# Optimization experiments

Measured on AMD Instinct MI355X. Metric: run time of the kernel, lower is better.

Reference implementation:

```python
import jax, jax.numpy as jnp
import numpy as np

E = 768      # embed_size
H = 12       # num_heads inside each nn.MultiheadAttention
G = 4        # num_groups
D = E // H   # per-head dim = 64


def setup_inputs() -> dict:
    key = jax.random.key(0)
    ks = jax.random.split(key, 20)
    s = 0.02
    B, S = 2, 2048
    inp = {
        "query": jax.random.normal(ks[0], (B, S, E), jnp.float32),
        "key":   jax.random.normal(ks[1], (B, S, E), jnp.float32),
        "value": jax.random.normal(ks[2], (B, S, E), jnp.float32),
        # outer projections (query_group_proj / key_proj / value_proj)
        "Wqg": jax.random.normal(ks[3], (E, E), jnp.float32) * s,
        "bqg": jnp.zeros((E,), jnp.float32),
        "Wk":  jax.random.normal(ks[4], (E, E), jnp.float32) * s,
        "bk":  jnp.zeros((E,), jnp.float32),
        "Wv":  jax.random.normal(ks[5], (E, E), jnp.float32) * s,
        "bv":  jnp.zeros((E,), jnp.float32),
        # per-group MultiheadAttention params (in_proj split into q/k/v, out_proj)
        "Wq_in": jax.random.normal(ks[6], (G, E, E), jnp.float32) * s,
        "bq_in": jnp.zeros((G, E), jnp.float32),
        "Wk_in": jax.random.normal(ks[7], (G, E, E), jnp.float32) * s,
        "bk_in": jnp.zeros((G, E), jnp.float32),
        "Wv_in": jax.random.normal(ks[8], (G, E, E), jnp.float32) * s,
        "bv_in": jnp.zeros((G, E), jnp.float32),
        "Wout":  jax.random.normal(ks[9], (G, E, E), jnp.float32) * s,
        "bout":  jnp.zeros((G, E), jnp.float32),
    }
    return inp


def reference(query, key, value, Wqg, bqg, Wk, bk, Wv, bv,
              Wq_in, bq_in, Wk_in, bk_in, Wv_in, bv_in, Wout, bout):
    B, S, _ = query.shape
    T = S // G  # tokens per group
    scale = 1.0 / np.sqrt(D).astype(np.float32)

    # outer projections (Linear: x @ W.T + b)
    q = query @ Wqg.T + bqg                         # [B,S,E]
    k = key   @ Wk.T  + bk                          # [B,S,E]
    v = value @ Wv.T  + bv                          # [B,S,E]

    # split query tokens into G interleaved groups (view + permute in source)
    qg = q.reshape(B, T, G, E).transpose(0, 2, 1, 3)  # [B,G,T,E]

    # per-group MHA input projections (batched over groups)
    qi = jnp.einsum('bgte,gfe->bgtf', qg, Wq_in) + bq_in[None, :, None, :]
    ki = jnp.einsum('bse,gfe->bgsf', k,  Wk_in) + bk_in[None, :, None, :]
    vi = jnp.einsum('bse,gfe->bgsf', v,  Wv_in) + bv_in[None, :, None, :]

    qh = qi.reshape(B, G, T, H, D)
    kh = ki.reshape(B, G, S, H, D)
    vh = vi.reshape(B, G, S, H, D)

    scores = jnp.einsum('bgthd,bgshd->bghts', qh, kh) * scale  # [B,G,H,T,S]
    attn = jax.nn.softmax(scores, axis=-1)
    ctx = jnp.einsum('bghts,bgshd->bgthd', attn, vh).reshape(B, G, T, E)

    out_g = jnp.einsum('bgte,gfe->bgtf', ctx, Wout) + bout[None, :, None, :]  # [B,G,T,E]

    # reassemble sequence order (inverse of the grouping permutation)
    out = out_g.transpose(0, 2, 1, 3).reshape(B, S, E)
    return out
```

## Files before the change

### kernel.cpp

```cpp
#include <hip/hip_runtime.h>
#include <hip/hip_bf16.h>


typedef __attribute__((ext_vector_type(8))) short short8;
typedef __attribute__((ext_vector_type(4))) float floatx4;

static __device__ __forceinline__ short f2bf(float f) {
    __bf16 b = (__bf16)f;
    return __builtin_bit_cast(short, b);
}
static __device__ __forceinline__ short8 f8_to_bf8(floatx4 f0, floatx4 f1) {
    short8 s;
    s[0]=f2bf(f0[0]); s[1]=f2bf(f0[1]); s[2]=f2bf(f0[2]); s[3]=f2bf(f0[3]);
    s[4]=f2bf(f1[0]); s[5]=f2bf(f1[1]); s[6]=f2bf(f1[2]); s[7]=f2bf(f1[3]);
    return s;
}
static __device__ __forceinline__ void gload_lds16(const short* g, short* l) {
    __builtin_amdgcn_global_load_lds(
        (const __attribute__((address_space(1))) unsigned int*)g,
        (__attribute__((address_space(3))) unsigned int*)l, 16, 0, 0);
}

__global__ __launch_bounds__(256) void cast_w(
    const float* a0, const float* a1, const float* a2, const float* a3,
    const float* a4, const float* a5, const float* a6, short* dst)
{
    const long U = 589824L;
    const float* ptrs[7] = {a0,a1,a2,a3,a4,a5,a6};
    const long starts[8] = {0, U, 2*U, 3*U, 7*U, 11*U, 15*U, 19*U};
    long i = (long)blockIdx.x * 2048 + (long)threadIdx.x * 8;
    int t = 0;
    while (t < 6 && i >= starts[t + 1]) t++;
    const float* s = ptrs[t] + (i - starts[t]);
    floatx4 f0 = *(const floatx4*)s;
    floatx4 f1 = *(const floatx4*)(s + 4);
    *(short8*)(dst + i) = f8_to_bf8(f0, f1);
}

#define GEMM_LANE_VARS                                                        \
    const int tid = threadIdx.x, lane = tid & 63, w = tid >> 6;               \
    const int wm = w & 1, wn = w >> 1;                                        \
    const int qr = lane >> 4, lc = lane & 15, x7 = lc & 7;                    \
    const int srow = tid >> 3, schunk = tid & 7, sx = srow & 7;

template<int CMODE, int BIAS_MODE>
static __device__ __forceinline__ void gemm_epilogue(
    floatx4 (&acc)[4][4], const float* bp, void* Cv, int ldc, int bm, int bn,
    int wm, int wn, int qr, int lc)
{
#pragma unroll
    for (int ni = 0; ni < 4; ni++) {
        const int gcol = bn * 128 + wn * 64 + ni * 16 + lc;
        const float bcol = (BIAS_MODE == 0) ? bp[gcol] : 0.f;
#pragma unroll
        for (int mi = 0; mi < 4; mi++) {
#pragma unroll
            for (int r = 0; r < 4; r++) {
                const int grow = bm * 128 + wm * 64 + mi * 16 + qr * 4 + r;
                const float bb = (BIAS_MODE == 1) ? bp[grow] : bcol;
                const float v = acc[mi][ni][r] + bb;
                if (CMODE == 0)
                    ((short*)Cv)[(long)grow * ldc + gcol] = f2bf(v);
                else
                    ((float*)Cv)[(long)grow * ldc + gcol] = v;
            }
        }
    }
}

static __device__ __forceinline__ void gemm_mfma_step(
    floatx4 (&acc)[4][4], const short* Ac, const short* Bc,
    int wm, int wn, int qr, int lc, int x7)
{
#pragma unroll
    for (int ks = 0; ks < 64; ks += 32) {
        const int c0 = (ks >> 3) + qr;
        const int slot = ((c0 ^ x7) << 3);
        short8 af[4], bfr[4];
#pragma unroll
        for (int mi = 0; mi < 4; mi++)
            af[mi] = *(const short8*)&Ac[(wm * 64 + mi * 16 + lc) * 64 + slot];
#pragma unroll
        for (int ni = 0; ni < 4; ni++)
            bfr[ni] = *(const short8*)&Bc[(wn * 64 + ni * 16 + lc) * 64 + slot];
#pragma unroll
        for (int mi = 0; mi < 4; mi++)
#pragma unroll
            for (int ni = 0; ni < 4; ni++)
                acc[mi][ni] = __builtin_amdgcn_mfma_f32_16x16x32_bf16(
                    af[mi], bfr[ni], acc[mi][ni], 0, 0, 0);
    }
}

template<int CMODE, int BIAS_MODE>
static __device__ __forceinline__ void gemm_core_db(
    const short* __restrict__ A, const short* __restrict__ Wb,
    const float* __restrict__ bp, void* __restrict__ Cv,
    int lda, int ldc, int bm, int bn, short* As, short* Bs)
{
    GEMM_LANE_VARS
    const short* Ab = A + (long)(bm * 128) * lda;
    const short* Wt = Wb + (long)(bn * 128) * 768;
    const int gch = ((schunk ^ sx) << 3);

    floatx4 acc[4][4];
#pragma unroll
    for (int mi = 0; mi < 4; mi++)
#pragma unroll
        for (int ni = 0; ni < 4; ni++) acc[mi][ni] = (floatx4){0.f, 0.f, 0.f, 0.f};

#pragma unroll
    for (int p = 0; p < 4; p++) {
        gload_lds16(Ab + (long)(p * 32 + srow) * lda + gch, &As[(p * 32 + w * 8) * 64]);
        gload_lds16(Wt + (long)(p * 32 + srow) * 768 + gch, &Bs[(p * 32 + w * 8) * 64]);
    }

    for (int kk = 0; kk < 12; kk++) {
        __syncthreads();
        if (kk < 11) {
            const int k1 = (kk + 1) * 64;
            const int nb = ((kk + 1) & 1) * 8192;
#pragma unroll
            for (int p = 0; p < 4; p++) {
                gload_lds16(Ab + (long)(p * 32 + srow) * lda + k1 + gch,
                            &As[nb + (p * 32 + w * 8) * 64]);
                gload_lds16(Wt + (long)(p * 32 + srow) * 768 + k1 + gch,
                            &Bs[nb + (p * 32 + w * 8) * 64]);
            }
        }
        gemm_mfma_step(acc, As + (kk & 1) * 8192, Bs + (kk & 1) * 8192,
                       wm, wn, qr, lc, x7);
    }
    gemm_epilogue<CMODE, BIAS_MODE>(acc, bp, Cv, ldc, bm, bn, wm, wn, qr, lc);
}

template<int CMODE, int BIAS_MODE>
static __device__ __forceinline__ void gemm_core_f32(
    const float* __restrict__ A, const short* __restrict__ Wb,
    const float* __restrict__ bp, void* __restrict__ Cv,
    int lda, int ldc, int bm, int bn, short* As, short* Bs)
{
    GEMM_LANE_VARS
    const short* Wt = Wb + (long)(bn * 128) * 768;

    floatx4 acc[4][4];
#pragma unroll
    for (int mi = 0; mi < 4; mi++)
#pragma unroll
        for (int ni = 0; ni < 4; ni++) acc[mi][ni] = (floatx4){0.f, 0.f, 0.f, 0.f};

    for (int k0 = 0; k0 < 768; k0 += 64) {
        __syncthreads();
#pragma unroll
        for (int p = 0; p < 4; p++) {
            const int row = p * 32 + srow;
            const float* ap = A + (long)(bm * 128 + row) * lda + k0 + schunk * 8;
            floatx4 f0 = *(const floatx4*)ap;
            floatx4 f1 = *(const floatx4*)(ap + 4);
            *(short8*)&As[row * 64 + ((schunk ^ sx) << 3)] = f8_to_bf8(f0, f1);
            gload_lds16(Wt + (long)row * 768 + k0 + ((schunk ^ sx) << 3),
                        &Bs[(p * 32 + w * 8) * 64]);
        }
        __syncthreads();
        gemm_mfma_step(acc, As, Bs, wm, wn, qr, lc, x7);
    }
    gemm_epilogue<CMODE, BIAS_MODE>(acc, bp, Cv, ldc, bm, bn, wm, wn, qr, lc);
}

__global__ __launch_bounds__(256) void qkv_gemm(
    const float* q, const float* k, const float* v, const short* Wbf,
    const float* bq, const float* bk, const float* bv, short* outp)
{
    __shared__ short As[128 * 64];
    __shared__ short Bs[128 * 64];
    const int xcd = blockIdx.x & 7, slot = blockIdx.x >> 3;
    const int bm = xcd * 4 + slot / 18;
    const int rem = slot % 18, y = rem / 6, bn = rem % 6;
    const float* A    = (y == 0) ? q  : (y == 1) ? k  : v;
    const float* bias = (y == 0) ? bq : (y == 1) ? bk : bv;
    gemm_core_f32<0, 0>(A, Wbf + (long)y * 589824, bias, outp + (long)y * 3145728,
                        768, 768, bm, bn, As, Bs);
}

template<int BIAS_MODE>
static __device__ __forceinline__ void gemm256_core(
    const short* __restrict__ A, const short* __restrict__ B,
    const float* __restrict__ bias, short* __restrict__ C,
    int lda, int ldc, int bm, int bn, short* As, short* Bs)
{
    const int tid = threadIdx.x, lane = tid & 63, w = tid >> 6;
    const int wm = w & 1, wn = w >> 1;
    const int qr = lane >> 4, lc = lane & 15, x7 = lc & 7;
    const int srow = tid >> 3, schunk = tid & 7;
    const int gch = ((schunk ^ (srow & 7)) << 3);

    const short* Ab = A + (long)(bm * 256) * lda;
    const short* Bb = B + (long)(bn * 256) * 768;

    floatx4 acc[8][4];
#pragma unroll
    for (int i = 0; i < 8; i++)
#pragma unroll
        for (int j = 0; j < 4; j++) acc[i][j] = (floatx4){0.f, 0.f, 0.f, 0.f};

#pragma unroll
    for (int r = 0; r < 256; r += 64) {
        gload_lds16(Ab + (long)(r + srow) * lda + gch, As + (r + w * 8) * 64);
        gload_lds16(Bb + (long)(r + srow) * 768 + gch, Bs + (r + w * 8) * 64);
    }

#pragma unroll 1
    for (int kt = 0; kt < 12; ++kt) {
        const int s = kt & 1;
        const short* Ac = As + s * 16384;
        const short* Bc = Bs + s * 16384;
        short* Ad = As + (1 - s) * 16384;
        short* Bd = Bs + (1 - s) * 16384;
        const int koff = (kt + 1) * 64;

        asm volatile("s_waitcnt vmcnt(0)" ::: "memory");
        __builtin_amdgcn_s_barrier();

        short8 af[4][2], bfr[2][2];
#pragma unroll
        for (int ph = 0; ph < 4; ++ph) {
            const int mh = ph >> 1, nh = ph & 1;
            if (nh == 0) {
#pragma unroll
                for (int mi = 0; mi < 4; mi++)
#pragma unroll
                    for (int ks = 0; ks < 2; ks++)
                        af[mi][ks] = *(const short8*)&Ac[
                            (wm * 128 + (mh * 4 + mi) * 16 + lc) * 64 +
                            ((((ks << 2) + qr) ^ x7) << 3)];
            }
#pragma unroll
            for (int ni = 0; ni < 2; ni++)
#pragma unroll
                for (int ks = 0; ks < 2; ks++)
                    bfr[ni][ks] = *(const short8*)&Bc[
                        (wn * 64 + (nh * 2 + ni) * 16 + lc) * 64 +
                        ((((ks << 2) + qr) ^ x7) << 3)];
            if (kt < 11) {
                const int r = ph * 64;
                gload_lds16(Ab + (long)(r + srow) * lda + koff + gch,
                            Ad + (r + w * 8) * 64);
                gload_lds16(Bb + (long)(r + srow) * 768 + koff + gch,
                            Bd + (r + w * 8) * 64);
            }
            __builtin_amdgcn_s_barrier();
            asm volatile("s_waitcnt lgkmcnt(0)" ::: "memory");
            __builtin_amdgcn_sched_barrier(0);
            __builtin_amdgcn_s_setprio(1);
#pragma unroll
            for (int ks = 0; ks < 2; ks++)
#pragma unroll
                for (int mi = 0; mi < 4; mi++)
#pragma unroll
                    for (int ni = 0; ni < 2; ni++)
                        acc[mh * 4 + mi][nh * 2 + ni] =
                            __builtin_amdgcn_mfma_f32_16x16x32_bf16(
                                af[mi][ks], bfr[ni][ks],
                                acc[mh * 4 + mi][nh * 2 + ni], 0, 0, 0);
            __builtin_amdgcn_s_setprio(0);
            __builtin_amdgcn_sched_barrier(0);
            __builtin_amdgcn_s_barrier();
        }
    }

#pragma unroll
    for (int ni = 0; ni < 4; ni++) {
        const int gcol = bn * 256 + wn * 64 + ni * 16 + lc;
        const float bcol = (BIAS_MODE == 0) ? bias[gcol] : 0.f;
#pragma unroll
        for (int mi = 0; mi < 8; mi++) {
#pragma unroll
            for (int r = 0; r < 4; r++) {
                const int grow = bm * 256 + wm * 128 + mi * 16 + qr * 4 + r;
                const float bb = (BIAS_MODE == 1) ? bias[grow] : bcol;
                C[(long)grow * ldc + gcol] = f2bf(acc[mi][ni][r] + bb);
            }
        }
    }
}

__global__ __launch_bounds__(512, 2) void mid_gemm2(
    const short* kproj, const short* vproj, const short* qproj, const short* Wbf,
    const float* bq_in, const float* bk_in, const float* bv_in,
    short* kiB, short* vtB, short* qiB)
{
    __shared__ short As[2 * 16384];
    __shared__ short Bs[2 * 16384];
    const int xcd = blockIdx.x & 7, slot = blockIdx.x >> 3;
    const int z = xcd, b = z >> 2, g = z & 3;
    if (slot < 24) {
        gemm256_core<0>(kproj + (long)b * 1572864, Wbf + (long)(7 + g) * 589824,
                        bk_in + g * 768, kiB + (long)z * 1572864,
                        768, 768, slot / 3, slot % 3, As, Bs);
    } else if (slot < 48) {
        const int s2 = slot - 24;
        gemm256_core<1>(Wbf + (long)(11 + g) * 589824, vproj + (long)b * 1572864,
                        bv_in + g * 768, vtB + (long)z * 1572864,
                        768, 2048, s2 / 8, s2 % 8, As, Bs);
    } else {
        const int s3 = slot - 48;
        gemm256_core<0>(qproj + (long)b * 1572864 + g * 768, Wbf + (long)(3 + g) * 589824,
                        bq_in + g * 768, qiB + (long)z * 393216,
                        3072, 768, s3 / 3, s3 % 3, As, Bs);
    }
}

__global__ __launch_bounds__(256) void out_gemm(
    const short* ctxB, const short* Wbf, const float* bout, float* out)
{
    extern __shared__ short sm[];
    short* As = sm;
    short* Bs = sm + 16384;
    const int xcd = blockIdx.x & 7, slot = blockIdx.x >> 3;
    const int z = xcd, b = z >> 2, g = z & 3;
    gemm_core_db<2, 0>(ctxB + (long)z * 393216, Wbf + (long)(15 + g) * 589824,
                       bout + g * 768, out + (long)b * 1572864 + g * 768,
                       768, 3072, slot / 6, slot % 6, As, Bs);
}

__global__ __launch_bounds__(256) void attn_kernel(
    const short* __restrict__ qi, const short* __restrict__ ki,
    const short* __restrict__ vt, short* __restrict__ ctx)
{
    __shared__ short Kt[2][64 * 64];
    __shared__ short Vt[2][64 * 64];
    __shared__ short Ps[4][16 * 64];

    const int tid = threadIdx.x, lane = tid & 63, w = tid >> 6;
    const int qr = lane >> 4, lc = lane & 15, x7 = lc & 7;
    const int headid = blockIdx.x % 96;
    const int tile = blockIdx.x / 96;
    const int h = headid % 12, bg = headid / 12;

    const short* qp = qi + ((long)bg * 512 + tile * 64 + w * 16 + lc) * 768 + h * 64 + qr * 8;
    const short8 aq0 = *(const short8*)qp;
    const short8 aq1 = *(const short8*)(qp + 32);

    const short one = (lc == 0) ? (short)0x3F80 : (short)0;
    const short8 onesv = (short8){one, one, one, one, one, one, one, one};

    floatx4 cacc[4], lacc = (floatx4){0.f, 0.f, 0.f, 0.f};
#pragma unroll
    for (int dc = 0; dc < 4; dc++) cacc[dc] = (floatx4){0.f, 0.f, 0.f, 0.f};

    const int srow = lane >> 3, schk = lane & 7, swz = schk ^ srow;
    const short* kgb = ki + ((long)bg * 2048) * 768 + h * 64;
    const short* vgb = vt + ((long)(bg * 768 + h * 64)) * 2048;

#pragma unroll
    for (int inst = 0; inst < 2; inst++) {
        const int rk = w * 16 + inst * 8 + srow;
        gload_lds16(kgb + (long)rk * 768 + swz * 8, &Kt[0][(w * 16 + inst * 8) * 64]);
        gload_lds16(vgb + (long)rk * 2048 + swz * 8, &Vt[0][(w * 16 + inst * 8) * 64]);
    }

    for (int it = 0; it < 32; it++) {
        const int cur = it & 1;
        __syncthreads();
        if (it < 31) {
            const int nxt = cur ^ 1, s0 = (it + 1) * 64;
#pragma unroll
            for (int inst = 0; inst < 2; inst++) {
                const int rk = w * 16 + inst * 8 + srow;
                gload_lds16(kgb + (long)(s0 + rk) * 768 + swz * 8,
                            &Kt[nxt][(w * 16 + inst * 8) * 64]);
                gload_lds16(vgb + (long)rk * 2048 + s0 + swz * 8,
                            &Vt[nxt][(w * 16 + inst * 8) * 64]);
            }
        }

        const short* Kb = &Kt[cur][0];
        const short* Vb = &Vt[cur][0];

        floatx4 sv[4];
#pragma unroll
        for (int ss = 0; ss < 4; ss++) {
            const short* kr = Kb + (ss * 16 + lc) * 64;
            short8 b0 = *(const short8*)(kr + ((qr ^ x7) << 3));
            short8 b1 = *(const short8*)(kr + (((4 + qr) ^ x7) << 3));
            floatx4 t = (floatx4){0.f, 0.f, 0.f, 0.f};
            t = __builtin_amdgcn_mfma_f32_16x16x32_bf16(aq0, b0, t, 0, 0, 0);
            t = __builtin_amdgcn_mfma_f32_16x16x32_bf16(aq1, b1, t, 0, 0, 0);
            sv[ss] = t;
        }

        short* ps = &Ps[w][0];
#pragma unroll
        for (int ss = 0; ss < 4; ss++) {
            const int cch = ss * 2 + (lc >> 3);
#pragma unroll
            for (int r = 0; r < 4; r++) {
                const int m = qr * 4 + r;
                ps[m * 64 + ((cch ^ (m & 7)) << 3) + x7] =
                    f2bf(__builtin_amdgcn_exp2f(sv[ss][r] * 0.18033688f));
            }
        }
        asm volatile("s_waitcnt lgkmcnt(0)" ::: "memory");
        const short8 ap0 = *(const short8*)&ps[lc * 64 + ((qr ^ x7) << 3)];
        const short8 ap1 = *(const short8*)&ps[lc * 64 + (((4 + qr) ^ x7) << 3)];

        lacc = __builtin_amdgcn_mfma_f32_16x16x32_bf16(ap0, onesv, lacc, 0, 0, 0);
        lacc = __builtin_amdgcn_mfma_f32_16x16x32_bf16(ap1, onesv, lacc, 0, 0, 0);
#pragma unroll
        for (int dc = 0; dc < 4; dc++) {
            const short* vr = Vb + (dc * 16 + lc) * 64;
            short8 bv0 = *(const short8*)(vr + ((qr ^ x7) << 3));
            short8 bv1 = *(const short8*)(vr + (((4 + qr) ^ x7) << 3));
            cacc[dc] = __builtin_amdgcn_mfma_f32_16x16x32_bf16(ap0, bv0, cacc[dc], 0, 0, 0);
            cacc[dc] = __builtin_amdgcn_mfma_f32_16x16x32_bf16(ap1, bv1, cacc[dc], 0, 0, 0);
        }
    }

    float linv[4];
#pragma unroll
    for (int r = 0; r < 4; r++)
        linv[r] = 1.f / __shfl(lacc[r], lane & 48);
    short* cp = ctx + ((long)bg * 512 + tile * 64 + w * 16) * 768 + h * 64;
#pragma unroll
    for (int dc = 0; dc < 4; dc++)
#pragma unroll
        for (int r = 0; r < 4; r++)
            cp[(qr * 4 + r) * 768 + dc * 16 + lc] = f2bf(cacc[dc][r] * linv[r]);
}

extern "C" void kernel_launch(void* const* d_in, const int* in_sizes, int n_in,
                              void* d_out, int out_size, void* d_ws, size_t ws_size,
                              hipStream_t stream) {
    const float* query = (const float*)d_in[0];
    const float* key   = (const float*)d_in[1];
    const float* value = (const float*)d_in[2];
    const float* Wqg = (const float*)d_in[3];  const float* bqg = (const float*)d_in[4];
    const float* Wk  = (const float*)d_in[5];  const float* bk  = (const float*)d_in[6];
    const float* Wv  = (const float*)d_in[7];  const float* bv  = (const float*)d_in[8];
    const float* Wq_in = (const float*)d_in[9];  const float* bq_in = (const float*)d_in[10];
    const float* Wk_in = (const float*)d_in[11]; const float* bk_in = (const float*)d_in[12];
    const float* Wv_in = (const float*)d_in[13]; const float* bv_in = (const float*)d_in[14];
    const float* Wout  = (const float*)d_in[15]; const float* bout  = (const float*)d_in[16];
    float* out = (float*)d_out;

    short* ws     = (short*)d_ws;
    short* Wbf    = ws;
    short* q_proj = ws + 11206656L;
    short* k_proj = ws + 14352384L;
    short* v_proj = ws + 17498112L;
    short* qiB    = ws + 20643840L;
    short* vtB    = ws + 23789568L;
    short* kiB    = ws + 36372480L;
    short* ctxB   = ws + 11206656L;

    dim3 blk(256);

    cast_w<<<dim3(5472), blk, 0, stream>>>(
        Wqg, Wk, Wv, Wq_in, Wk_in, Wv_in, Wout, Wbf);

    qkv_gemm<<<dim3(576), blk, 0, stream>>>(
        query, key, value, Wbf, bqg, bk, bv, q_proj);

    mid_gemm2<<<dim3(432), dim3(512), 0, stream>>>(
        k_proj, v_proj, q_proj, Wbf, bq_in, bk_in, bv_in, kiB, vtB, qiB);

    attn_kernel<<<dim3(768), blk, 0, stream>>>(qiB, kiB, vtB, ctxB);

    out_gemm<<<dim3(192), blk, 65536, stream>>>(ctxB, Wbf, bout, out);
}
```

Measured before the change: 306.1 us.

## Restructure 256x256 bf16 GEMM into 4-stage 32-wide K pipeline with new LDS layout

Replaces the double-buffered 64-wide K tiles in the mid-layer GEMM core with a four-slot ring of 32-wide K tiles, prefetching three steps ahead and using partial vmcnt waits instead of draining all loads each iteration. The LDS layout changes to an MFMA-fragment-friendly row pairing with a new XOR swizzle, so each lane reads one short8 per fragment. The aim is to hide global-to-LDS latency better and cut full-drain stalls, at the cost of twice as many loop iterations and barriers.

```diff
diff --git a/kernel.cpp b/kernel.cpp
--- a/kernel.cpp
+++ b/kernel.cpp
@@ -190,9 +190,11 @@
 {
     const int tid = threadIdx.x, lane = tid & 63, w = tid >> 6;
     const int wm = w & 1, wn = w >> 1;
-    const int qr = lane >> 4, lc = lane & 15, x7 = lc & 7;
-    const int srow = tid >> 3, schunk = tid & 7;
-    const int gch = ((schunk ^ (srow & 7)) << 3);
+    const int qr = lane >> 4, lc = lane & 15;
+    const int Rrel = 2 * (lane >> 3) + ((lane >> 2) & 1);
+    const int kq8  = (((lane & 3) ^ ((lane >> 3) & 3)) << 3);
+    const int rhalf = lc >> 1;
+    const int rbase = ((lc & 1) << 5) + ((qr ^ (rhalf & 3)) << 3);
 
     const short* Ab = A + (long)(bm * 256) * lda;
     const short* Bb = B + (long)(bn * 256) * 768;
@@ -203,70 +205,69 @@
 #pragma unroll
         for (int j = 0; j < 4; j++) acc[i][j] = (floatx4){0.f, 0.f, 0.f, 0.f};
 
-#pragma unroll
-    for (int r = 0; r < 256; r += 64) {
-        gload_lds16(Ab + (long)(r + srow) * lda + gch, As + (r + w * 8) * 64);
-        gload_lds16(Bb + (long)(r + srow) * 768 + gch, Bs + (r + w * 8) * 64);
-    }
+#define STG_A(j, i)                                                           \
+    gload_lds16(Ab + (long)(16 * (w + 8 * (i)) + Rrel) * lda + (j) * 32 + kq8,\
+                As + ((j) & 3) * 8192 + (w + 8 * (i)) * 512)
+#define STG_B(j, i)                                                           \
+    gload_lds16(Bb + (long)(16 * (w + 8 * (i)) + Rrel) * 768 + (j) * 32 + kq8,\
+                Bs + ((j) & 3) * 8192 + (w + 8 * (i)) * 512)
+
+    STG_A(0, 0); STG_A(0, 1); STG_B(0, 0); STG_B(0, 1);
+    STG_A(1, 0); STG_A(1, 1); STG_B(1, 0); STG_B(1, 1);
+    STG_A(2, 0); STG_A(2, 1); STG_B(2, 0); STG_B(2, 1);
+    asm volatile("s_waitcnt vmcnt(8)" ::: "memory");
+    __builtin_amdgcn_s_barrier();
 
 #pragma unroll 1
-    for (int kt = 0; kt < 12; ++kt) {
-        const int s = kt & 1;
-        const short* Ac = As + s * 16384;
-        const short* Bc = Bs + s * 16384;
-        short* Ad = As + (1 - s) * 16384;
-        short* Bd = Bs + (1 - s) * 16384;
-        const int koff = (kt + 1) * 64;
-
-        asm volatile("s_waitcnt vmcnt(0)" ::: "memory");
+    for (int j = 0; j < 24; ++j) {
+        const short* Ac = As + (j & 3) * 8192;
+        const short* Bc = Bs + (j & 3) * 8192;
+        short8 af[4], bf[4];
+
+#pragma unroll
+        for (int ni = 0; ni < 4; ni++)
+            bf[ni] = *(const short8*)&Bc[(wn * 32 + ni * 8 + rhalf) * 64 + rbase];
+#pragma unroll
+        for (int mi = 0; mi < 4; mi++)
+            af[mi] = *(const short8*)&Ac[(wm * 64 + mi * 8 + rhalf) * 64 + rbase];
+        if (j <= 20) { STG_A(j + 3, 0); STG_A(j + 3, 1); }
         __builtin_amdgcn_s_barrier();
-
-        short8 af[4][2], bfr[2][2];
-#pragma unroll
-        for (int ph = 0; ph < 4; ++ph) {
-            const int mh = ph >> 1, nh = ph & 1;
-            if (nh == 0) {
-#pragma unroll
-                for (int mi = 0; mi < 4; mi++)
-#pragma unroll
-                    for (int ks = 0; ks < 2; ks++)
-                        af[mi][ks] = *(const short8*)&Ac[
-                            (wm * 128 + (mh * 4 + mi) * 16 + lc) * 64 +
-                            ((((ks << 2) + qr) ^ x7) << 3)];
-            }
-#pragma unroll
-            for (int ni = 0; ni < 2; ni++)
-#pragma unroll
-                for (int ks = 0; ks < 2; ks++)
-                    bfr[ni][ks] = *(const short8*)&Bc[
-                        (wn * 64 + (nh * 2 + ni) * 16 + lc) * 64 +
-                        ((((ks << 2) + qr) ^ x7) << 3)];
-            if (kt < 11) {
-                const int r = ph * 64;
-                gload_lds16(Ab + (long)(r + srow) * lda + koff + gch,
-                            Ad + (r + w * 8) * 64);
-                gload_lds16(Bb + (long)(r + srow) * 768 + koff + gch,
-                            Bd + (r + w * 8) * 64);
-            }
-            __builtin_amdgcn_s_barrier();
-            asm volatile("s_waitcnt lgkmcnt(0)" ::: "memory");
-            __builtin_amdgcn_sched_barrier(0);
-            __builtin_amdgcn_s_setprio(1);
-#pragma unroll
-            for (int ks = 0; ks < 2; ks++)
-#pragma unroll
-                for (int mi = 0; mi < 4; mi++)
-#pragma unroll
-                    for (int ni = 0; ni < 2; ni++)
-                        acc[mh * 4 + mi][nh * 2 + ni] =
-                            __builtin_amdgcn_mfma_f32_16x16x32_bf16(
-                                af[mi][ks], bfr[ni][ks],
-                                acc[mh * 4 + mi][nh * 2 + ni], 0, 0, 0);
-            __builtin_amdgcn_s_setprio(0);
-            __builtin_amdgcn_sched_barrier(0);
-            __builtin_amdgcn_s_barrier();
-        }
-    }
+        asm volatile("s_waitcnt lgkmcnt(0)" ::: "memory");
+        __builtin_amdgcn_sched_barrier(0);
+        __builtin_amdgcn_s_setprio(1);
+#pragma unroll
+        for (int mi = 0; mi < 4; mi++)
+#pragma unroll
+            for (int ni = 0; ni < 4; ni++)
+                acc[mi][ni] = __builtin_amdgcn_mfma_f32_16x16x32_bf16(
+                    af[mi], bf[ni], acc[mi][ni], 0, 0, 0);
+        __builtin_amdgcn_s_setprio(0);
+        __builtin_amdgcn_sched_barrier(0);
+        __builtin_amdgcn_s_barrier();
+
+#pragma unroll
+        for (int mi = 0; mi < 4; mi++)
+            af[mi] = *(const short8*)&Ac[(wm * 64 + 32 + mi * 8 + rhalf) * 64 + rbase];
+        if (j <= 20) { STG_B(j + 3, 0); STG_B(j + 3, 1); }
+        __builtin_amdgcn_s_barrier();
+        asm volatile("s_waitcnt lgkmcnt(0)" ::: "memory");
+        __builtin_amdgcn_sched_barrier(0);
+        __builtin_amdgcn_s_setprio(1);
+#pragma unroll
+        for (int mi = 0; mi < 4; mi++)
+#pragma unroll
+            for (int ni = 0; ni < 4; ni++)
+                acc[4 + mi][ni] = __builtin_amdgcn_mfma_f32_16x16x32_bf16(
+                    af[mi], bf[ni], acc[4 + mi][ni], 0, 0, 0);
+        __builtin_amdgcn_s_setprio(0);
+        __builtin_amdgcn_sched_barrier(0);
+        if (j <= 20)      asm volatile("s_waitcnt vmcnt(8)" ::: "memory");
+        else if (j == 21) asm volatile("s_waitcnt vmcnt(4)" ::: "memory");
+        else              asm volatile("s_waitcnt vmcnt(0)" ::: "memory");
+        __builtin_amdgcn_s_barrier();
+    }
+#undef STG_A
+#undef STG_B
 
 #pragma unroll
     for (int ni = 0; ni < 4; ni++) {
@@ -289,8 +290,8 @@
     const float* bq_in, const float* bk_in, const float* bv_in,
     short* kiB, short* vtB, short* qiB)
 {
-    __shared__ short As[2 * 16384];
-    __shared__ short Bs[2 * 16384];
+    __shared__ __align__(16) short As[4 * 8192];
+    __shared__ __align__(16) short Bs[4 * 8192];
     const int xcd = blockIdx.x & 7, slot = blockIdx.x >> 3;
     const int z = xcd, b = z >> 2, g = z & 3;
     if (slot < 24) {
```

Measured after the change: 310.2 us. Within noise of the previous version (+1.3%).
